# Performance work log

Measured on AMD Instinct MI355X. Metric: run time of the kernel, lower is better.

## Reference

```python
import jax, jax.numpy as jnp
import numpy as np

# Problem dims
M, K, N = 16384, 1024, 1024
# QuantParams baked as constants (Python scalars in the original module)
INPUT_SCALE, INPUT_ZP = 0.05, 3
WEIGHT_SCALE, WEIGHT_ZP = 0.02, 0
OUTPUT_SCALE, OUTPUT_ZP = 0.1, -5
QMIN, QMAX = -128, 127
# round(combined_scale * 1024) computed in Python, exactly as in the torch module
SCALE_INT = round(INPUT_SCALE * WEIGHT_SCALE / OUTPUT_SCALE * 1024)  # = 10


def setup_inputs() -> dict:
    key = jax.random.key(0)
    k1, k2, k3 = jax.random.split(key, 3)
    x = jax.random.randint(k1, (M, K), -128, 128, dtype=jnp.int32).astype(jnp.int8)
    weight_int = jax.random.randint(k2, (N, K), -128, 128, dtype=jnp.int32).astype(jnp.int8)
    bias_int = jax.random.randint(k3, (N,), -1000, 1000, dtype=jnp.int32)
    return {"x": x, "weight_int": weight_int, "bias_int": bias_int}


def reference(x, weight_int, bias_int):
    # F.linear(x.int32 - input_zp, W.int32 - weight_zp, bias_int)
    xi = x.astype(jnp.int32) - INPUT_ZP            # [M, K] int32
    wi = weight_int.astype(jnp.int32) - WEIGHT_ZP  # [N, K] int32
    acc = jnp.matmul(xi, wi.T) + bias_int          # [M, N] int32 accumulate
    # integer requant: (acc * scale_int) // 1024 in int64 (torch // is floor div,
    # matching jnp floor_divide semantics)
    res = (acc.astype(jnp.int64) * SCALE_INT) // 1024
    res = jnp.clip(res + OUTPUT_ZP, QMIN, QMAX)
    return res.astype(jnp.int8)
```

## Files before the change

kernel.cpp:

```cpp
#include <hip/hip_runtime.h>
#include <stdint.h>

#define M_DIM 16384
#define N_DIM 1024
#define K_DIM 1024

#define BM 128
#define BN 128
#define BK 64
#define NKT (K_DIM / BK)
#define TILE_BYTES (BM * BK)

using i32x4 = __attribute__((ext_vector_type(4))) int;

__device__ __forceinline__ int pack4(int4 v) {
    return (v.x & 0xFF) | ((v.y & 0xFF) << 8) | ((v.z & 0xFF) << 16) | ((v.w & 0xFF) << 24);
}


__global__ __launch_bounds__(256) void pack_x_kernel(const int* __restrict__ X,
                                                     int8_t* __restrict__ xqT) {
    int mtile = blockIdx.x >> 4;
    int kt = blockIdx.x & 15;
    int8_t* outT = xqT + (size_t)blockIdx.x * TILE_BYTES;
    int tid = threadIdx.x;
#pragma unroll
    for (int i = 0; i < 2; ++i) {
        int c = i * 256 + tid;
        int row = c >> 2;
        int sig = c & 3;
        const int* src = X + ((size_t)(mtile * BM + row)) * K_DIM + kt * BK + sig * 16;
        int4 p;
        p.x = pack4(*(const int4*)(src + 0));
        p.y = pack4(*(const int4*)(src + 4));
        p.z = pack4(*(const int4*)(src + 8));
        p.w = pack4(*(const int4*)(src + 12));
        int s = sig ^ ((row >> 1) & 3);
        *(int4*)(outT + ((size_t)row * 4 + s) * 16) = p;
    }
}

__global__ __launch_bounds__(256) void pack_w_corr_kernel(const int* __restrict__ w,
                                                          const int* __restrict__ bias,
                                                          int8_t* __restrict__ wqT,
                                                          int* __restrict__ corr) {
    int n = blockIdx.x;
    int t = threadIdx.x;
    int4 v = ((const int4*)(w + (size_t)n * K_DIM))[t];
    int pk = pack4(v);
    int kt = t >> 4;
    int sig = (t >> 2) & 3;
    int d = t & 3;
    int rowin = n & 127;
    int ntile = n >> 7;
    int s = sig ^ ((rowin >> 1) & 3);
    ((int*)(wqT + ((size_t)(ntile * NKT + kt)) * TILE_BYTES))[(rowin * 4 + s) * 4 + d] = pk;

    int sum = v.x + v.y + v.z + v.w;
#pragma unroll
    for (int m = 1; m < 64; m <<= 1) sum += __shfl_xor(sum, m);
    __shared__ int partial[4];
    if ((t & 63) == 0) partial[t >> 6] = sum;
    __syncthreads();
    if (t == 0)
        corr[n] = bias[n] - 3 * (partial[0] + partial[1] + partial[2] + partial[3]);
}

__global__ __launch_bounds__(256) void gemm_kernel(const int8_t* __restrict__ xqT,
                                                   const int8_t* __restrict__ wqT,
                                                   const int* __restrict__ corr,
                                                   int* __restrict__ out) {
    __shared__ int8_t Asm[TILE_BYTES];
    __shared__ int8_t Bsm[TILE_BYTES];

    int bid = blockIdx.x;
    int swz = (bid & 7) * 128 + (bid >> 3);
    int mtile = swz >> 3;
    int ntile = swz & 7;
    int n0 = ntile * BN;

    int tid = threadIdx.x;
    int lane = tid & 63;
    int wave = tid >> 6;
    int wm = wave >> 1;
    int wn = wave & 1;
    int r16 = lane & 15;
    int krow = lane >> 4;
    int slot = krow ^ ((r16 >> 1) & 3);

    i32x4 acc[4][4];
#pragma unroll
    for (int i = 0; i < 4; ++i)
#pragma unroll
        for (int j = 0; j < 4; ++j)
            acc[i][j] = (i32x4){0, 0, 0, 0};

    const int8_t* Abase = xqT + (size_t)mtile * NKT * TILE_BYTES;
    const int8_t* Bbase = wqT + (size_t)ntile * NKT * TILE_BYTES;

    for (int kt = 0; kt < NKT; ++kt) {
        const int8_t* Ag = Abase + (size_t)kt * TILE_BYTES;
        const int8_t* Bg = Bbase + (size_t)kt * TILE_BYTES;
#pragma unroll
        for (int i = 0; i < 2; ++i) {
            int f = i * 256 + tid;
            __builtin_amdgcn_global_load_lds(
                (const __attribute__((address_space(1))) unsigned int*)(Ag + (size_t)f * 16),
                (__attribute__((address_space(3))) unsigned int*)(Asm + f * 16),
                16, 0, 0);
        }
#pragma unroll
        for (int i = 0; i < 2; ++i) {
            int f = i * 256 + tid;
            __builtin_amdgcn_global_load_lds(
                (const __attribute__((address_space(1))) unsigned int*)(Bg + (size_t)f * 16),
                (__attribute__((address_space(3))) unsigned int*)(Bsm + f * 16),
                16, 0, 0);
        }
        __syncthreads();

        i32x4 afr[4], bfr[4];
#pragma unroll
        for (int i = 0; i < 4; ++i) {
            afr[i] = *(const i32x4*)(Asm + (size_t)(wm * 64 + i * 16 + r16) * 64 + slot * 16);
            bfr[i] = *(const i32x4*)(Bsm + (size_t)(wn * 64 + i * 16 + r16) * 64 + slot * 16);
        }
#pragma unroll
        for (int i = 0; i < 4; ++i)
#pragma unroll
            for (int j = 0; j < 4; ++j)
                acc[i][j] = __builtin_amdgcn_mfma_i32_16x16x64_i8(afr[i], bfr[j], acc[i][j], 0, 0, 0);
        __syncthreads();
    }

    int m0 = mtile * BM;
    int col16 = lane & 15;
    int rbase = (lane >> 4) * 4;
#pragma unroll
    for (int j = 0; j < 4; ++j) {
        int c = n0 + wn * 64 + j * 16 + col16;
        int cr = corr[c];
#pragma unroll
        for (int i = 0; i < 4; ++i) {
            int rrow = m0 + wm * 64 + i * 16 + rbase;
#pragma unroll
            for (int r = 0; r < 4; ++r) {
                int t = acc[i][j][r] + cr;
                int res = ((t * 10) >> 10) - 5;
                res = res < -128 ? -128 : (res > 127 ? 127 : res);
                out[(size_t)(rrow + r) * N_DIM + c] = res;
            }
        }
    }
}

extern "C" void kernel_launch(void* const* d_in, const int* in_sizes, int n_in,
                              void* d_out, int out_size, void* d_ws, size_t ws_size,
                              hipStream_t stream) {
    (void)in_sizes; (void)n_in; (void)out_size; (void)ws_size;
    const int* x    = (const int*)d_in[0];
    const int* w    = (const int*)d_in[1];
    const int* bias = (const int*)d_in[2];
    int* out = (int*)d_out;

    int8_t* xqT = (int8_t*)d_ws;
    int8_t* wqT = xqT + (size_t)M_DIM * K_DIM;
    int* corr   = (int*)(wqT + (size_t)N_DIM * K_DIM);

    pack_x_kernel<<<(M_DIM / BM) * NKT, 256, 0, stream>>>(x, xqT);
    pack_w_corr_kernel<<<N_DIM, 256, 0, stream>>>(w, bias, wqT, corr);
    gemm_kernel<<<(M_DIM / BM) * (N_DIM / BN), 256, 0, stream>>>(xqT, wqT, corr, out);
}
```

Baseline: 136.4 us.

## Double-buffer LDS tiles to overlap global loads with MFMA compute

```diff
diff --git a/kernel.cpp b/kernel.cpp
--- a/kernel.cpp
+++ b/kernel.cpp
@@ -70,8 +70,8 @@
                                                    const int8_t* __restrict__ wqT,
                                                    const int* __restrict__ corr,
                                                    int* __restrict__ out) {
-    __shared__ int8_t Asm[TILE_BYTES];
-    __shared__ int8_t Bsm[TILE_BYTES];
+    __shared__ int8_t Asm[2][TILE_BYTES];
+    __shared__ int8_t Bsm[2][TILE_BYTES];
 
     int bid = blockIdx.x;
     int swz = (bid & 7) * 128 + (bid >> 3);
@@ -98,57 +98,73 @@
     const int8_t* Abase = xqT + (size_t)mtile * NKT * TILE_BYTES;
     const int8_t* Bbase = wqT + (size_t)ntile * NKT * TILE_BYTES;
 
+#define STAGE(buf, kt)                                                                     \
+    {                                                                                      \
+        const int8_t* Ag = Abase + (size_t)(kt) * TILE_BYTES;                              \
+        const int8_t* Bg = Bbase + (size_t)(kt) * TILE_BYTES;                              \
+        _Pragma("unroll") for (int i = 0; i < 2; ++i) {                                    \
+            int f = i * 256 + tid;                                                         \
+            __builtin_amdgcn_global_load_lds(                                              \
+                (const __attribute__((address_space(1))) unsigned int*)(Ag + (size_t)f * 16), \
+                (__attribute__((address_space(3))) unsigned int*)(&Asm[buf][0] + f * 16),  \
+                16, 0, 0);                                                                 \
+        }                                                                                  \
+        _Pragma("unroll") for (int i = 0; i < 2; ++i) {                                    \
+            int f = i * 256 + tid;                                                         \
+            __builtin_amdgcn_global_load_lds(                                              \
+                (const __attribute__((address_space(1))) unsigned int*)(Bg + (size_t)f * 16), \
+                (__attribute__((address_space(3))) unsigned int*)(&Bsm[buf][0] + f * 16),  \
+                16, 0, 0);                                                                 \
+        }                                                                                  \
+    }
+
+    STAGE(0, 0);
+
+#pragma unroll
     for (int kt = 0; kt < NKT; ++kt) {
-        const int8_t* Ag = Abase + (size_t)kt * TILE_BYTES;
-        const int8_t* Bg = Bbase + (size_t)kt * TILE_BYTES;
-#pragma unroll
-        for (int i = 0; i < 2; ++i) {
-            int f = i * 256 + tid;
-            __builtin_amdgcn_global_load_lds(
-                (const __attribute__((address_space(1))) unsigned int*)(Ag + (size_t)f * 16),
-                (__attribute__((address_space(3))) unsigned int*)(Asm + f * 16),
-                16, 0, 0);
+        const int cur = kt & 1;
+        if (kt < NKT - 1) {
+            STAGE(cur ^ 1, kt + 1);
+            asm volatile("s_waitcnt vmcnt(4)" ::: "memory");
+        } else {
+            asm volatile("s_waitcnt vmcnt(0)" ::: "memory");
         }
-#pragma unroll
-        for (int i = 0; i < 2; ++i) {
-            int f = i * 256 + tid;
-            __builtin_amdgcn_global_load_lds(
-                (const __attribute__((address_space(1))) unsigned int*)(Bg + (size_t)f * 16),
-                (__attribute__((address_space(3))) unsigned int*)(Bsm + f * 16),
-                16, 0, 0);
-        }
-        __syncthreads();
+        __builtin_amdgcn_s_barrier();
 
         i32x4 afr[4], bfr[4];
 #pragma unroll
         for (int i = 0; i < 4; ++i) {
-            afr[i] = *(const i32x4*)(Asm + (size_t)(wm * 64 + i * 16 + r16) * 64 + slot * 16);
-            bfr[i] = *(const i32x4*)(Bsm + (size_t)(wn * 64 + i * 16 + r16) * 64 + slot * 16);
+            afr[i] = *(const i32x4*)(&Asm[cur][0] + (size_t)(wm * 64 + i * 16 + r16) * 64 + slot * 16);
+            bfr[i] = *(const i32x4*)(&Bsm[cur][0] + (size_t)(wn * 64 + i * 16 + r16) * 64 + slot * 16);
         }
 #pragma unroll
         for (int i = 0; i < 4; ++i)
 #pragma unroll
             for (int j = 0; j < 4; ++j)
                 acc[i][j] = __builtin_amdgcn_mfma_i32_16x16x64_i8(afr[i], bfr[j], acc[i][j], 0, 0, 0);
-        __syncthreads();
+
+        if (kt < NKT - 1) __builtin_amdgcn_s_barrier();
     }
+#undef STAGE
 
     int m0 = mtile * BM;
     int col16 = lane & 15;
     int rbase = (lane >> 4) * 4;
+    int cr[4];
 #pragma unroll
-    for (int j = 0; j < 4; ++j) {
-        int c = n0 + wn * 64 + j * 16 + col16;
-        int cr = corr[c];
+    for (int j = 0; j < 4; ++j) cr[j] = corr[n0 + wn * 64 + j * 16 + col16];
 #pragma unroll
-        for (int i = 0; i < 4; ++i) {
-            int rrow = m0 + wm * 64 + i * 16 + rbase;
+    for (int i = 0; i < 4; ++i) {
+        int rrow = m0 + wm * 64 + i * 16 + rbase;
 #pragma unroll
-            for (int r = 0; r < 4; ++r) {
-                int t = acc[i][j][r] + cr;
+        for (int r = 0; r < 4; ++r) {
+            size_t rowoff = (size_t)(rrow + r) * N_DIM;
+#pragma unroll
+            for (int j = 0; j < 4; ++j) {
+                int t = acc[i][j][r] + cr[j];
                 int res = ((t * 10) >> 10) - 5;
                 res = res < -128 ? -128 : (res > 127 ? 127 : res);
-                out[(size_t)(rrow + r) * N_DIM + c] = res;
+                out[rowoff + n0 + wn * 64 + j * 16 + col16] = res;
             }
         }
     }
```

After: 140.0 us. 1.03x slower.
